# Kernel tuning notes

Measured on AMD Instinct MI355X. Metric: run time of the kernel, lower is better.

The kernel has to match this reference:

```python
import jax, jax.numpy as jnp
import numpy as np

N = 50000   # nodes
E = 800000  # edges
IN = 256    # input feature dim
H = 4       # heads (per layer)
D = 64      # num_hidden per head
C = 16      # n_clusters
NEG = 0.2   # leaky_relu negative slope


def _gat_conv(x, W, attn_l, attn_r, src, dst):
    """DGL GATConv (no residual, no dropout at eval), activation=elu.
    x: [N, F_in], W: [F_in, H*D], attn_l/attn_r: [H, D]. Returns [N, H, D]."""
    feat = (x @ W).reshape(N, H, D)                      # [N,H,D]
    el = jnp.sum(feat * attn_l, axis=-1)                 # [N,H]
    er = jnp.sum(feat * attn_r, axis=-1)                 # [N,H]
    e = jax.nn.leaky_relu(el[src] + er[dst], NEG)        # [E,H]
    # numerically stable segment softmax over incoming edges of each dst node
    emax = jax.ops.segment_max(e, dst, num_segments=N)   # [N,H]
    emax = jnp.where(jnp.isfinite(emax), emax, 0.0)
    ee = jnp.exp(e - emax[dst])                          # [E,H]
    denom = jax.ops.segment_sum(ee, dst, num_segments=N) # [N,H]
    a = ee / jnp.maximum(denom[dst], 1e-9)               # [E,H]
    msg = feat[src] * a[:, :, None]                      # [E,H,D]
    rst = jax.ops.segment_sum(msg, dst, num_segments=N)  # [N,H,D]
    return jax.nn.elu(rst)


def setup_inputs() -> dict:
    key = jax.random.key(0)
    ks = jax.random.split(key, 12)
    def w(k, shape, fan):
        return jax.random.normal(k, shape, jnp.float32) * np.float32(1.0 / np.sqrt(fan))
    return {
        "x": jax.random.normal(ks[0], (N, IN), jnp.float32),
        "src": jax.random.randint(ks[1], (E,), 0, N, jnp.int32),
        "dst": jax.random.randint(ks[2], (E,), 0, N, jnp.int32),
        "W0": w(ks[3], (IN, H * D), IN),
        "al0": w(ks[4], (H, D), D),
        "ar0": w(ks[5], (H, D), D),
        "W1": w(ks[6], (H * D, H * D), H * D),
        "al1": w(ks[7], (H, D), D),
        "ar1": w(ks[8], (H, D), D),
        "Wc": w(ks[9], (D, C), D),
        "bc": jnp.zeros((C,), jnp.float32),
    }


def reference(x, src, dst, W0, al0, ar0, W1, al1, ar1, Wc, bc):
    h = _gat_conv(x, W0, al0, ar0, src, dst)              # [N,H,D]
    h = _gat_conv(h.reshape(N, H * D), W1, al1, ar1, src, dst)
    heads = jnp.transpose(h, (1, 0, 2))                   # [H,N,D]
    # original bug: same cluster layer (index num_layers-1) used for every head
    cs = jax.nn.softmax(jnp.einsum("hnd,dc->hnc", heads, Wc) + bc, axis=-1)  # [H,N,C]
    # pack (heads, cs) into one array along last dim for a single output
    return jnp.concatenate([heads, cs], axis=-1)          # [H,N,D+C]
```

## Files before the change

kernel.cpp:

```cpp
#include <hip/hip_runtime.h>
#include <hip/hip_bf16.h>
#include <math.h>

#define N_NODES 50000
#define N_EDGES 800000
#define NH 4
#define ND 64
#define NF 256
#define NC 16
#define NEG_SLOPE 0.2f

typedef __attribute__((ext_vector_type(8))) short bf16x8;
typedef __attribute__((ext_vector_type(4))) float f32x4;

__device__ __forceinline__ float elu_f(float x) {
    return x > 0.f ? x : (__expf(x) - 1.f);
}

__device__ __forceinline__ ushort bf16_rne(float f) {
    union { float f; unsigned u; } v; v.f = f;
    unsigned u = v.u;
    u += 0x7fffu + ((u >> 16) & 1u);
    return (ushort)(u >> 16);
}

__device__ __forceinline__ float bf2f(ushort u) {
    return __uint_as_float(((unsigned)u) << 16);
}

__global__ __launch_bounds__(256) void cast_bf16_kernel(const float* __restrict__ in,
                                                        ushort* __restrict__ out, int n8) {
    int i = blockIdx.x * 256 + threadIdx.x;
    if (i >= n8) return;
    float4 a = *(const float4*)(in + i * 8);
    float4 b = *(const float4*)(in + i * 8 + 4);
    ushort o[8] = {bf16_rne(a.x), bf16_rne(a.y), bf16_rne(a.z), bf16_rne(a.w),
                   bf16_rne(b.x), bf16_rne(b.y), bf16_rne(b.z), bf16_rne(b.w)};
    *(bf16x8*)(out + i * 8) = *(bf16x8*)o;
}

__global__ __launch_bounds__(256) void castWt_kernel(const float* __restrict__ W0,
                                                     const float* __restrict__ W1,
                                                     ushort* __restrict__ Wt0,
                                                     ushort* __restrict__ Wt1) {
    const float* W = (blockIdx.x < 256) ? W0 : W1;
    ushort* Wt = (blockIdx.x < 256) ? Wt0 : Wt1;
    int n = blockIdx.x & 255;
    int k = threadIdx.x;
    Wt[n * 256 + k] = bf16_rne(W[k * 256 + n]);
}

__global__ __launch_bounds__(256) void gemm_bf16(const ushort* __restrict__ A,
                                                 const ushort* __restrict__ Bt,
                                                 ushort* __restrict__ Cbf,
                                                 const float* __restrict__ al,
                                                 const float* __restrict__ ar,
                                                 float* __restrict__ el,
                                                 float* __restrict__ er, int M) {
    __shared__ __align__(16) ushort As[128 * 64];
    __shared__ __align__(16) ushort Bs[128 * 64];
    const int t = threadIdx.x;
    const int l = t & 63;
    const int w = t >> 6;
    const int wm = (w >> 1) * 64, wn = (w & 1) * 64;
    const int m0 = blockIdx.x * 128, n0 = blockIdx.y * 128;
    const int lr = l & 15, lk = l >> 4;

    f32x4 acc[4][4] = {};
    const int sr = t >> 3;
    const int sc = t & 7;
    const int scw = sc ^ (sr & 7);

    for (int k0 = 0; k0 < 256; k0 += 64) {
        #pragma unroll
        for (int q = 0; q < 4; ++q) {
            int row = q * 32 + sr;
            int ga = min(m0 + row, M - 1);
            bf16x8 va = *(const bf16x8*)(A + (size_t)ga * 256 + k0 + sc * 8);
            *(bf16x8*)(&As[row * 64 + scw * 8]) = va;
            bf16x8 vb = *(const bf16x8*)(Bt + (size_t)(n0 + row) * 256 + k0 + sc * 8);
            *(bf16x8*)(&Bs[row * 64 + scw * 8]) = vb;
        }
        __syncthreads();
        #pragma unroll
        for (int kk = 0; kk < 2; ++kk) {
            bf16x8 af[4], bfr[4];
            #pragma unroll
            for (int mi = 0; mi < 4; ++mi) {
                int row = wm + mi * 16 + lr;
                int kb = kk * 4 + lk;
                af[mi] = *(const bf16x8*)(&As[row * 64 + (kb ^ (row & 7)) * 8]);
            }
            #pragma unroll
            for (int ni = 0; ni < 4; ++ni) {
                int col = wn + ni * 16 + lr;
                int kb = kk * 4 + lk;
                bfr[ni] = *(const bf16x8*)(&Bs[col * 64 + (kb ^ (col & 7)) * 8]);
            }
            #pragma unroll
            for (int mi = 0; mi < 4; ++mi)
                #pragma unroll
                for (int ni = 0; ni < 4; ++ni)
                    acc[mi][ni] = __builtin_amdgcn_mfma_f32_16x16x32_bf16(af[mi], bfr[ni], acc[mi][ni], 0, 0, 0);
        }
        __syncthreads();
    }
    const int h = (n0 + wn) >> 6;
    float alv[4], arv[4];
    #pragma unroll
    for (int ni = 0; ni < 4; ++ni) {
        alv[ni] = al[h * ND + ni * 16 + lr];
        arv[ni] = ar[h * ND + ni * 16 + lr];
    }
    #pragma unroll
    for (int mi = 0; mi < 4; ++mi) {
        #pragma unroll
        for (int j = 0; j < 4; ++j) {
            int row = m0 + wm + mi * 16 + lk * 4 + j;
            float pe = 0.f, pr = 0.f;
            #pragma unroll
            for (int ni = 0; ni < 4; ++ni) {
                float v = acc[mi][ni][j];
                pe += v * alv[ni];
                pr += v * arv[ni];
                if (row < M)
                    Cbf[(size_t)row * 256 + n0 + wn + ni * 16 + lr] = bf16_rne(v);
            }
            #pragma unroll
            for (int m = 1; m <= 8; m <<= 1) {
                pe += __shfl_xor(pe, m, 64);
                pr += __shfl_xor(pr, m, 64);
            }
            if (lr == 0 && row < M) {
                el[row * 4 + h] = pe;
                er[row * 4 + h] = pr;
            }
        }
    }
}

__global__ __launch_bounds__(256) void hist_kernel(const int* __restrict__ dst, int* __restrict__ count) {
    int e = blockIdx.x * 256 + threadIdx.x;
    if (e < N_EDGES) atomicAdd(&count[dst[e]], 1);
}

__global__ __launch_bounds__(256) void scan1_kernel(const int* __restrict__ counts,
                                                    int* __restrict__ offs,
                                                    int* __restrict__ bsums) {
    __shared__ int sh[256];
    int tid = threadIdx.x;
    int i = blockIdx.x * 256 + tid;
    int v = (i < N_NODES) ? counts[i] : 0;
    sh[tid] = v;
    __syncthreads();
    #pragma unroll
    for (int ofs = 1; ofs < 256; ofs <<= 1) {
        int t = (tid >= ofs) ? sh[tid - ofs] : 0;
        __syncthreads();
        sh[tid] += t;
        __syncthreads();
    }
    if (i < N_NODES) offs[i] = sh[tid] - v;
    if (tid == 255) bsums[blockIdx.x] = sh[255];
}

__global__ __launch_bounds__(256) void scan2_kernel(const int* __restrict__ bsums,
                                                    int* __restrict__ boffs, int nb) {
    __shared__ int sh[256];
    int tid = threadIdx.x;
    int v = (tid < nb) ? bsums[tid] : 0;
    sh[tid] = v;
    __syncthreads();
    #pragma unroll
    for (int ofs = 1; ofs < 256; ofs <<= 1) {
        int t = (tid >= ofs) ? sh[tid - ofs] : 0;
        __syncthreads();
        sh[tid] += t;
        __syncthreads();
    }
    if (tid < nb) boffs[tid] = sh[tid] - v;
}

__global__ __launch_bounds__(256) void scan3_kernel(int* __restrict__ offs,
                                                    const int* __restrict__ boffs,
                                                    int* __restrict__ cursor) {
    int i = blockIdx.x * 256 + threadIdx.x;
    if (i < N_NODES) {
        int v = offs[i] + boffs[i >> 8];
        offs[i] = v;
        cursor[i] = v;
    }
    if (i == 0) offs[N_NODES] = N_EDGES;
}

__global__ __launch_bounds__(256) void scatter_kernel(const int* __restrict__ src,
                                                      const int* __restrict__ dst,
                                                      int* __restrict__ cursor,
                                                      int* __restrict__ csrc,
                                                      int* __restrict__ cdst) {
    int e = blockIdx.x * 256 + threadIdx.x;
    if (e >= N_EDGES) return;
    int d = dst[e];
    int p = atomicAdd(&cursor[d], 1);
    csrc[p] = src[e];
    cdst[p] = d;
}

__global__ __launch_bounds__(256) void edge_w_kernel(const int* __restrict__ csrc,
                                                     const int* __restrict__ cdst,
                                                     const float* __restrict__ el,
                                                     const float* __restrict__ er,
                                                     float* __restrict__ w) {
    int i = blockIdx.x * 256 + threadIdx.x;
    if (i >= N_EDGES) return;
    int s = csrc[i], d = cdst[i];
    float4 lv = *(const float4*)(el + s * 4);
    float4 rv = *(const float4*)(er + d * 4);
    float lvv[4] = {lv.x, lv.y, lv.z, lv.w};
    float rvv[4] = {rv.x, rv.y, rv.z, rv.w};
    float o[4];
    #pragma unroll
    for (int hh = 0; hh < 4; ++hh) {
        float v = lvv[hh] + rvv[hh];
        v = v > 0.f ? v : NEG_SLOPE * v;
        o[hh] = __expf(v);
    }
    *(float4*)(w + (size_t)i * 4) = make_float4(o[0], o[1], o[2], o[3]);
}

#define AGG_BATCH16()                                                            \
    for (int i = s0; i < s1; i += 16) {                                          \
        int sid[16]; float wv[16]; ushort4 fr[16];                               \
        _Pragma("unroll")                                                        \
        for (int u = 0; u < 16; ++u) {                                           \
            int idx = (i + u < s1) ? i + u : s1 - 1;                             \
            sid[u] = csrc[idx];                                                  \
            wv[u] = (i + u < s1) ? w[(size_t)idx * 4 + h] : 0.f;                 \
        }                                                                        \
        _Pragma("unroll")                                                        \
        for (int u = 0; u < 16; ++u)                                             \
            fr[u] = *(const ushort4*)(featbf + (size_t)sid[u] * NF + lane * 4);  \
        _Pragma("unroll")                                                        \
        for (int u = 0; u < 16; ++u) {                                           \
            dsum += wv[u];                                                       \
            acc.x += wv[u] * bf2f(fr[u].x);                                      \
            acc.y += wv[u] * bf2f(fr[u].y);                                      \
            acc.z += wv[u] * bf2f(fr[u].z);                                      \
            acc.w += wv[u] * bf2f(fr[u].w);                                      \
        }                                                                        \
    }

__global__ __launch_bounds__(256) void agg_l0_kernel(const ushort* __restrict__ featbf,
                                                     const int* __restrict__ csrc,
                                                     const int* __restrict__ offs,
                                                     const float* __restrict__ w,
                                                     ushort* __restrict__ out_bf) {
    int n = blockIdx.x * 4 + (threadIdx.x >> 6);
    int lane = threadIdx.x & 63;
    int h = lane >> 4;
    int s0 = offs[n], s1 = offs[n + 1];
    float4 acc = make_float4(0.f, 0.f, 0.f, 0.f);
    float dsum = 0.f;
    AGG_BATCH16()
    float inv = 1.f / fmaxf(dsum, 1e-9f);
    ushort o[4] = {bf16_rne(elu_f(acc.x * inv)), bf16_rne(elu_f(acc.y * inv)),
                   bf16_rne(elu_f(acc.z * inv)), bf16_rne(elu_f(acc.w * inv))};
    *(ushort4*)(out_bf + (size_t)n * NF + lane * 4) = *(ushort4*)o;
}

__global__ __launch_bounds__(256) void agg_final_kernel(const ushort* __restrict__ featbf,
                                                        const int* __restrict__ csrc,
                                                        const int* __restrict__ offs,
                                                        const float* __restrict__ w,
                                                        const float* __restrict__ Wc,
                                                        const float* __restrict__ bc,
                                                        float* __restrict__ out) {
    int n = blockIdx.x * 4 + (threadIdx.x >> 6);
    int lane = threadIdx.x & 63;
    int h = lane >> 4;
    int g = lane & 15;
    int s0 = offs[n], s1 = offs[n + 1];
    float4 acc = make_float4(0.f, 0.f, 0.f, 0.f);
    float dsum = 0.f;
    AGG_BATCH16()
    float inv = 1.f / fmaxf(dsum, 1e-9f);
    float v0 = elu_f(acc.x * inv), v1 = elu_f(acc.y * inv);
    float v2 = elu_f(acc.z * inv), v3 = elu_f(acc.w * inv);
    size_t base = (size_t)h * N_NODES * (ND + NC) + (size_t)n * (ND + NC);
    *(float4*)(out + base + g * 4) = make_float4(v0, v1, v2, v3);
    float logit[NC];
    #pragma unroll
    for (int c = 0; c < NC; ++c) {
        int d0 = g * 4;
        float p = v0 * Wc[(d0 + 0) * NC + c] + v1 * Wc[(d0 + 1) * NC + c] +
                  v2 * Wc[(d0 + 2) * NC + c] + v3 * Wc[(d0 + 3) * NC + c];
        p += __shfl_xor(p, 1, 64);
        p += __shfl_xor(p, 2, 64);
        p += __shfl_xor(p, 4, 64);
        p += __shfl_xor(p, 8, 64);
        logit[c] = p + bc[c];
    }
    float m = logit[0];
    #pragma unroll
    for (int c = 1; c < NC; ++c) m = fmaxf(m, logit[c]);
    float ssum = 0.f;
    #pragma unroll
    for (int c = 0; c < NC; ++c) ssum += __expf(logit[c] - m);
    out[base + ND + g] = __expf(logit[g] - m) / ssum;
}

extern "C" void kernel_launch(void* const* d_in, const int* in_sizes, int n_in,
                              void* d_out, int out_size, void* d_ws, size_t ws_size,
                              hipStream_t stream) {
    const float* x   = (const float*)d_in[0];
    const int* src   = (const int*)d_in[1];
    const int* dst   = (const int*)d_in[2];
    const float* W0  = (const float*)d_in[3];
    const float* al0 = (const float*)d_in[4];
    const float* ar0 = (const float*)d_in[5];
    const float* W1  = (const float*)d_in[6];
    const float* al1 = (const float*)d_in[7];
    const float* ar1 = (const float*)d_in[8];
    const float* Wc  = (const float*)d_in[9];
    const float* bc  = (const float*)d_in[10];
    float* out = (float*)d_out;

    char* ws = (char*)d_ws;
    size_t off = 0;
    auto alloc = [&](size_t bytes) { void* p = ws + off; off = (off + bytes + 255) & ~(size_t)255; return p; };
    ushort* featbf = (ushort*)alloc((size_t)N_NODES * NF * 2);
    ushort* xbf    = (ushort*)alloc((size_t)N_NODES * NF * 2);
    ushort* hbuf   = (ushort*)alloc((size_t)N_NODES * NF * 2);
    ushort* Wt0    = (ushort*)alloc((size_t)256 * 256 * 2);
    ushort* Wt1    = (ushort*)alloc((size_t)256 * 256 * 2);
    float*  el     = (float*)alloc((size_t)N_NODES * NH * 4);
    float*  er     = (float*)alloc((size_t)N_NODES * NH * 4);
    float*  wbuf   = (float*)alloc((size_t)N_EDGES * NH * 4);
    int* counts    = (int*)alloc((size_t)N_NODES * 4);
    int* offs      = (int*)alloc((size_t)(N_NODES + 1) * 4);
    int* cursor    = (int*)alloc((size_t)N_NODES * 4);
    int* csrc      = (int*)alloc((size_t)N_EDGES * 4);
    int* cdst      = (int*)alloc((size_t)N_EDGES * 4);
    int* bsums     = (int*)alloc(256 * 4);
    int* boffs     = (int*)alloc(256 * 4);

    const int EB = (N_EDGES + 255) / 256;
    const int NB = (N_NODES + 255) / 256;
    const int GEMM_MB = (N_NODES + 127) / 128;
    const int C8 = (N_NODES * NF / 8 + 255) / 256;

    hipMemsetAsync(counts, 0, (size_t)N_NODES * 4, stream);
    hist_kernel<<<EB, 256, 0, stream>>>(dst, counts);
    scan1_kernel<<<NB, 256, 0, stream>>>(counts, offs, bsums);
    scan2_kernel<<<1, 256, 0, stream>>>(bsums, boffs, NB);
    scan3_kernel<<<NB, 256, 0, stream>>>(offs, boffs, cursor);
    scatter_kernel<<<EB, 256, 0, stream>>>(src, dst, cursor, csrc, cdst);

    castWt_kernel<<<512, 256, 0, stream>>>(W0, W1, Wt0, Wt1);
    cast_bf16_kernel<<<C8, 256, 0, stream>>>(x, xbf, N_NODES * NF / 8);

    gemm_bf16<<<dim3(GEMM_MB, 2), 256, 0, stream>>>(xbf, Wt0, featbf, al0, ar0, el, er, N_NODES);
    edge_w_kernel<<<EB, 256, 0, stream>>>(csrc, cdst, el, er, wbuf);
    agg_l0_kernel<<<N_NODES / 4, 256, 0, stream>>>(featbf, csrc, offs, wbuf, hbuf);

    gemm_bf16<<<dim3(GEMM_MB, 2), 256, 0, stream>>>(hbuf, Wt1, featbf, al1, ar1, el, er, N_NODES);
    edge_w_kernel<<<EB, 256, 0, stream>>>(csrc, cdst, el, er, wbuf);
    agg_final_kernel<<<N_NODES / 4, 256, 0, stream>>>(featbf, csrc, offs, wbuf, Wc, bc, out);
}
```

Before: 380.0 us.

## Stage gathered neighbor feature rows through LDS via global_load_lds in aggregation

The aggregation kernels now gather neighbor feature rows with direct global-to-LDS 16-byte loads instead of per-lane 8-byte register loads. Each instruction fetches two source rows, with half the wave on each row, into a per-wave LDS buffer. The row is then read back from LDS for accumulation. Node index and edge offsets are made wave-uniform with readfirstlane. The aim is wider memory transactions and lower VGPR pressure. The cost is an extra LDS round trip, a full vmcnt(0) wait per chunk, and 32KB of LDS per block, which may reduce occupancy.

```diff
diff --git a/kernel.cpp b/kernel.cpp
--- a/kernel.cpp
+++ b/kernel.cpp
@@ -9,6 +9,7 @@
 #define NF 256
 #define NC 16
 #define NEG_SLOPE 0.2f
+#define AGG_CHUNK 16
 
 typedef __attribute__((ext_vector_type(8))) short bf16x8;
 typedef __attribute__((ext_vector_type(4))) float f32x4;
@@ -26,6 +27,13 @@
 
 __device__ __forceinline__ float bf2f(ushort u) {
     return __uint_as_float(((unsigned)u) << 16);
+}
+
+__device__ __forceinline__ void row_pair_to_lds(const ushort* gp, char* lp) {
+    __builtin_amdgcn_global_load_lds(
+        (const __attribute__((address_space(1))) unsigned int*)gp,
+        (__attribute__((address_space(3))) unsigned int*)lp,
+        16, 0, 0);
 }
 
 __global__ __launch_bounds__(256) void cast_bf16_kernel(const float* __restrict__ in,
@@ -228,26 +236,33 @@
     *(float4*)(w + (size_t)i * 4) = make_float4(o[0], o[1], o[2], o[3]);
 }
 
-#define AGG_BATCH16()                                                            \
-    for (int i = s0; i < s1; i += 16) {                                          \
-        int sid[16]; float wv[16]; ushort4 fr[16];                               \
-        _Pragma("unroll")                                                        \
-        for (int u = 0; u < 16; ++u) {                                           \
-            int idx = (i + u < s1) ? i + u : s1 - 1;                             \
-            sid[u] = csrc[idx];                                                  \
-            wv[u] = (i + u < s1) ? w[(size_t)idx * 4 + h] : 0.f;                 \
-        }                                                                        \
-        _Pragma("unroll")                                                        \
-        for (int u = 0; u < 16; ++u)                                             \
-            fr[u] = *(const ushort4*)(featbf + (size_t)sid[u] * NF + lane * 4);  \
-        _Pragma("unroll")                                                        \
-        for (int u = 0; u < 16; ++u) {                                           \
-            dsum += wv[u];                                                       \
-            acc.x += wv[u] * bf2f(fr[u].x);                                      \
-            acc.y += wv[u] * bf2f(fr[u].y);                                      \
-            acc.z += wv[u] * bf2f(fr[u].z);                                      \
-            acc.w += wv[u] * bf2f(fr[u].w);                                      \
-        }                                                                        \
+#define AGG_STAGE_LOOP()                                                          \
+    for (int i = s0; i < s1; i += AGG_CHUNK) {                                    \
+        int sid[AGG_CHUNK]; float wv[AGG_CHUNK];                                  \
+        _Pragma("unroll")                                                         \
+        for (int u = 0; u < AGG_CHUNK; ++u) {                                     \
+            int sl = i + u;                                                       \
+            int idx = sl < s1 ? sl : s1 - 1;                                      \
+            sid[u] = csrc[idx];                                                   \
+            wv[u] = sl < s1 ? w[(size_t)idx * 4 + h] : 0.f;                       \
+        }                                                                         \
+        _Pragma("unroll")                                                         \
+        for (int u = 0; u < AGG_CHUNK / 2; ++u) {                                 \
+            int s2 = rowsel ? sid[2 * u + 1] : sid[2 * u];                        \
+            const ushort* gp = featbf + (size_t)s2 * NF + bsub * 8;               \
+            row_pair_to_lds(gp, myl + u * 1024);                                  \
+        }                                                                         \
+        asm volatile("s_waitcnt vmcnt(0)" ::: "memory");                          \
+        __builtin_amdgcn_sched_barrier(0);                                        \
+        _Pragma("unroll")                                                         \
+        for (int u = 0; u < AGG_CHUNK; ++u) {                                     \
+            ushort4 fr = *(const ushort4*)(myl + u * 512 + lane * 8);             \
+            dsum += wv[u];                                                        \
+            acc.x += wv[u] * bf2f(fr.x);                                          \
+            acc.y += wv[u] * bf2f(fr.y);                                          \
+            acc.z += wv[u] * bf2f(fr.z);                                          \
+            acc.w += wv[u] * bf2f(fr.w);                                          \
+        }                                                                         \
     }
 
 __global__ __launch_bounds__(256) void agg_l0_kernel(const ushort* __restrict__ featbf,
@@ -255,13 +270,19 @@
                                                      const int* __restrict__ offs,
                                                      const float* __restrict__ w,
                                                      ushort* __restrict__ out_bf) {
-    int n = blockIdx.x * 4 + (threadIdx.x >> 6);
+    __shared__ __align__(16) char ldsbuf[4][AGG_CHUNK * 512];
+    int wid = threadIdx.x >> 6;
+    char* myl = &ldsbuf[wid][0];
+    int n = __builtin_amdgcn_readfirstlane(blockIdx.x * 4 + wid);
     int lane = threadIdx.x & 63;
     int h = lane >> 4;
-    int s0 = offs[n], s1 = offs[n + 1];
+    int rowsel = lane >> 5;
+    int bsub = lane & 31;
+    int s0 = __builtin_amdgcn_readfirstlane(offs[n]);
+    int s1 = __builtin_amdgcn_readfirstlane(offs[n + 1]);
     float4 acc = make_float4(0.f, 0.f, 0.f, 0.f);
     float dsum = 0.f;
-    AGG_BATCH16()
+    AGG_STAGE_LOOP()
     float inv = 1.f / fmaxf(dsum, 1e-9f);
     ushort o[4] = {bf16_rne(elu_f(acc.x * inv)), bf16_rne(elu_f(acc.y * inv)),
                    bf16_rne(elu_f(acc.z * inv)), bf16_rne(elu_f(acc.w * inv))};
@@ -275,14 +296,20 @@
                                                         const float* __restrict__ Wc,
                                                         const float* __restrict__ bc,
                                                         float* __restrict__ out) {
-    int n = blockIdx.x * 4 + (threadIdx.x >> 6);
+    __shared__ __align__(16) char ldsbuf[4][AGG_CHUNK * 512];
+    int wid = threadIdx.x >> 6;
+    char* myl = &ldsbuf[wid][0];
+    int n = __builtin_amdgcn_readfirstlane(blockIdx.x * 4 + wid);
     int lane = threadIdx.x & 63;
     int h = lane >> 4;
     int g = lane & 15;
-    int s0 = offs[n], s1 = offs[n + 1];
+    int rowsel = lane >> 5;
+    int bsub = lane & 31;
+    int s0 = __builtin_amdgcn_readfirstlane(offs[n]);
+    int s1 = __builtin_amdgcn_readfirstlane(offs[n + 1]);
     float4 acc = make_float4(0.f, 0.f, 0.f, 0.f);
     float dsum = 0.f;
-    AGG_BATCH16()
+    AGG_STAGE_LOOP()
     float inv = 1.f / fmaxf(dsum, 1e-9f);
     float v0 = elu_f(acc.x * inv), v1 = elu_f(acc.y * inv);
     float v2 = elu_f(acc.z * inv), v3 = elu_f(acc.w * inv);
```

Measured after the change: 440.1 us. +15.8%, slower.

## Slice feature matrix into 32-column planes for cache-local gather aggregation

Applied to the files above, without the earlier changes.

The GEMM now writes its bf16 output as 8 column slices of 32 features, each stored contiguously per node. Aggregation launches 8 blocks per node group, one per slice, so each block gathers 64-byte rows from a 3.2MB plane that can stay in L2/MALL instead of random 512-byte rows across the full matrix. Within a wave, lanes split into 8 edge groups and partial sums are reduced with shuffles. The cluster softmax is moved to a separate kernel that rereads the output. This costs 8x more index and weight reads, an extra launch and an extra pass over the output.

```diff
diff --git a/kernel.cpp b/kernel.cpp
--- a/kernel.cpp
+++ b/kernel.cpp
@@ -9,6 +9,8 @@
 #define NF 256
 #define NC 16
 #define NEG_SLOPE 0.2f
+#define NSLICE 8
+#define SLICE_W 32
 
 typedef __attribute__((ext_vector_type(8))) short bf16x8;
 typedef __attribute__((ext_vector_type(4))) float f32x4;
@@ -52,7 +54,7 @@
 
 __global__ __launch_bounds__(256) void gemm_bf16(const ushort* __restrict__ A,
                                                  const ushort* __restrict__ Bt,
-                                                 ushort* __restrict__ Cbf,
+                                                 ushort* __restrict__ Cs,
                                                  const float* __restrict__ al,
                                                  const float* __restrict__ ar,
                                                  float* __restrict__ el,
@@ -120,11 +122,12 @@
             float pe = 0.f, pr = 0.f;
             #pragma unroll
             for (int ni = 0; ni < 4; ++ni) {
+                int col = n0 + wn + ni * 16 + lr;
                 float v = acc[mi][ni][j];
                 pe += v * alv[ni];
                 pr += v * arv[ni];
                 if (row < M)
-                    Cbf[(size_t)row * 256 + n0 + wn + ni * 16 + lr] = bf16_rne(v);
+                    Cs[(size_t)(col >> 5) * N_NODES * SLICE_W + (size_t)row * SLICE_W + (col & 31)] = bf16_rne(v);
             }
             #pragma unroll
             for (int m = 1; m <= 8; m <<= 1) {
@@ -228,72 +231,85 @@
     *(float4*)(w + (size_t)i * 4) = make_float4(o[0], o[1], o[2], o[3]);
 }
 
-#define AGG_BATCH16()                                                            \
-    for (int i = s0; i < s1; i += 16) {                                          \
-        int sid[16]; float wv[16]; ushort4 fr[16];                               \
-        _Pragma("unroll")                                                        \
-        for (int u = 0; u < 16; ++u) {                                           \
-            int idx = (i + u < s1) ? i + u : s1 - 1;                             \
-            sid[u] = csrc[idx];                                                  \
-            wv[u] = (i + u < s1) ? w[(size_t)idx * 4 + h] : 0.f;                 \
-        }                                                                        \
-        _Pragma("unroll")                                                        \
-        for (int u = 0; u < 16; ++u)                                             \
-            fr[u] = *(const ushort4*)(featbf + (size_t)sid[u] * NF + lane * 4);  \
-        _Pragma("unroll")                                                        \
-        for (int u = 0; u < 16; ++u) {                                           \
-            dsum += wv[u];                                                       \
-            acc.x += wv[u] * bf2f(fr[u].x);                                      \
-            acc.y += wv[u] * bf2f(fr[u].y);                                      \
-            acc.z += wv[u] * bf2f(fr[u].z);                                      \
-            acc.w += wv[u] * bf2f(fr[u].w);                                      \
-        }                                                                        \
-    }
-
-__global__ __launch_bounds__(256) void agg_l0_kernel(const ushort* __restrict__ featbf,
-                                                     const int* __restrict__ csrc,
-                                                     const int* __restrict__ offs,
-                                                     const float* __restrict__ w,
-                                                     ushort* __restrict__ out_bf) {
-    int n = blockIdx.x * 4 + (threadIdx.x >> 6);
-    int lane = threadIdx.x & 63;
-    int h = lane >> 4;
-    int s0 = offs[n], s1 = offs[n + 1];
-    float4 acc = make_float4(0.f, 0.f, 0.f, 0.f);
-    float dsum = 0.f;
-    AGG_BATCH16()
+#define AGG_SLICE_BODY()                                                           \
+    int b = blockIdx.x;                                                            \
+    int slice = b & 7;                                                             \
+    int wid = threadIdx.x >> 6;                                                    \
+    int n = ((b >> 3) << 2) + wid;                                                 \
+    int lane = threadIdx.x & 63;                                                   \
+    int eg = lane >> 3, fc = lane & 7;                                             \
+    int h = slice >> 1;                                                            \
+    const ushort* base = fs + (size_t)slice * N_NODES * SLICE_W;                   \
+    int s0 = offs[n], s1 = offs[n + 1];                                            \
+    float4 acc = make_float4(0.f, 0.f, 0.f, 0.f);                                  \
+    float dsum = 0.f;                                                              \
+    for (int i = s0; i < s1; i += 16) {                                            \
+        int iA = i + eg, iB = i + 8 + eg;                                          \
+        int idxA = min(iA, s1 - 1), idxB = min(iB, s1 - 1);                        \
+        int sA = csrc[idxA], sB = csrc[idxB];                                      \
+        float wA = iA < s1 ? wbuf[(size_t)idxA * 4 + h] : 0.f;                     \
+        float wB = iB < s1 ? wbuf[(size_t)idxB * 4 + h] : 0.f;                     \
+        ushort4 fA = *(const ushort4*)(base + (size_t)sA * SLICE_W + fc * 4);      \
+        ushort4 fB = *(const ushort4*)(base + (size_t)sB * SLICE_W + fc * 4);      \
+        acc.x += wA * bf2f(fA.x) + wB * bf2f(fB.x);                                \
+        acc.y += wA * bf2f(fA.y) + wB * bf2f(fB.y);                                \
+        acc.z += wA * bf2f(fA.z) + wB * bf2f(fB.z);                                \
+        acc.w += wA * bf2f(fA.w) + wB * bf2f(fB.w);                                \
+        dsum += wA + wB;                                                           \
+    }                                                                              \
+    _Pragma("unroll")                                                              \
+    for (int m = 8; m <= 32; m <<= 1) {                                            \
+        acc.x += __shfl_xor(acc.x, m, 64);                                         \
+        acc.y += __shfl_xor(acc.y, m, 64);                                         \
+        acc.z += __shfl_xor(acc.z, m, 64);                                         \
+        acc.w += __shfl_xor(acc.w, m, 64);                                         \
+        dsum += __shfl_xor(dsum, m, 64);                                           \
+    }                                                                              \
     float inv = 1.f / fmaxf(dsum, 1e-9f);
-    ushort o[4] = {bf16_rne(elu_f(acc.x * inv)), bf16_rne(elu_f(acc.y * inv)),
-                   bf16_rne(elu_f(acc.z * inv)), bf16_rne(elu_f(acc.w * inv))};
-    *(ushort4*)(out_bf + (size_t)n * NF + lane * 4) = *(ushort4*)o;
-}
-
-__global__ __launch_bounds__(256) void agg_final_kernel(const ushort* __restrict__ featbf,
-                                                        const int* __restrict__ csrc,
-                                                        const int* __restrict__ offs,
-                                                        const float* __restrict__ w,
-                                                        const float* __restrict__ Wc,
-                                                        const float* __restrict__ bc,
-                                                        float* __restrict__ out) {
+
+__global__ __launch_bounds__(256) void agg_slice_l0(const ushort* __restrict__ fs,
+                                                    const int* __restrict__ csrc,
+                                                    const int* __restrict__ offs,
+                                                    const float* __restrict__ wbuf,
+                                                    ushort* __restrict__ hbuf) {
+    AGG_SLICE_BODY()
+    if (eg == 0) {
+        ushort o[4] = {bf16_rne(elu_f(acc.x * inv)), bf16_rne(elu_f(acc.y * inv)),
+                       bf16_rne(elu_f(acc.z * inv)), bf16_rne(elu_f(acc.w * inv))};
+        *(ushort4*)(hbuf + (size_t)n * NF + slice * SLICE_W + fc * 4) = *(ushort4*)o;
+    }
+}
+
+__global__ __launch_bounds__(256) void agg_slice_final(const ushort* __restrict__ fs,
+                                                       const int* __restrict__ csrc,
+                                                       const int* __restrict__ offs,
+                                                       const float* __restrict__ wbuf,
+                                                       float* __restrict__ out) {
+    AGG_SLICE_BODY()
+    if (eg == 0) {
+        float4 v = make_float4(elu_f(acc.x * inv), elu_f(acc.y * inv),
+                               elu_f(acc.z * inv), elu_f(acc.w * inv));
+        size_t p = (size_t)h * N_NODES * (ND + NC) + (size_t)n * (ND + NC)
+                 + (slice & 1) * SLICE_W + fc * 4;
+        *(float4*)(out + p) = v;
+    }
+}
+
+__global__ __launch_bounds__(256) void cluster_kernel(const float* __restrict__ Wc,
+                                                      const float* __restrict__ bc,
+                                                      float* __restrict__ out) {
     int n = blockIdx.x * 4 + (threadIdx.x >> 6);
     int lane = threadIdx.x & 63;
     int h = lane >> 4;
     int g = lane & 15;
-    int s0 = offs[n], s1 = offs[n + 1];
-    float4 acc = make_float4(0.f, 0.f, 0.f, 0.f);
-    float dsum = 0.f;
-    AGG_BATCH16()
-    float inv = 1.f / fmaxf(dsum, 1e-9f);
-    float v0 = elu_f(acc.x * inv), v1 = elu_f(acc.y * inv);
-    float v2 = elu_f(acc.z * inv), v3 = elu_f(acc.w * inv);
     size_t base = (size_t)h * N_NODES * (ND + NC) + (size_t)n * (ND + NC);
-    *(float4*)(out + base + g * 4) = make_float4(v0, v1, v2, v3);
+    float4 v = *(const float4*)(out + base + g * 4);
     float logit[NC];
     #pragma unroll
     for (int c = 0; c < NC; ++c) {
         int d0 = g * 4;
-        float p = v0 * Wc[(d0 + 0) * NC + c] + v1 * Wc[(d0 + 1) * NC + c] +
-                  v2 * Wc[(d0 + 2) * NC + c] + v3 * Wc[(d0 + 3) * NC + c];
+        float p = v.x * Wc[(d0 + 0) * NC + c] + v.y * Wc[(d0 + 1) * NC + c] +
+                  v.z * Wc[(d0 + 2) * NC + c] + v.w * Wc[(d0 + 3) * NC + c];
         p += __shfl_xor(p, 1, 64);
         p += __shfl_xor(p, 2, 64);
         p += __shfl_xor(p, 4, 64);
@@ -328,7 +344,7 @@
     char* ws = (char*)d_ws;
     size_t off = 0;
     auto alloc = [&](size_t bytes) { void* p = ws + off; off = (off + bytes + 255) & ~(size_t)255; return p; };
-    ushort* featbf = (ushort*)alloc((size_t)N_NODES * NF * 2);
+    ushort* featsl = (ushort*)alloc((size_t)N_NODES * NF * 2);
     ushort* xbf    = (ushort*)alloc((size_t)N_NODES * NF * 2);
     ushort* hbuf   = (ushort*)alloc((size_t)N_NODES * NF * 2);
     ushort* Wt0    = (ushort*)alloc((size_t)256 * 256 * 2);
@@ -348,6 +364,7 @@
     const int NB = (N_NODES + 255) / 256;
     const int GEMM_MB = (N_NODES + 127) / 128;
     const int C8 = (N_NODES * NF / 8 + 255) / 256;
+    const int AGG_B = (N_NODES / 4) * NSLICE;
 
     hipMemsetAsync(counts, 0, (size_t)N_NODES * 4, stream);
     hist_kernel<<<EB, 256, 0, stream>>>(dst, counts);
@@ -359,11 +376,13 @@
     castWt_kernel<<<512, 256, 0, stream>>>(W0, W1, Wt0, Wt1);
     cast_bf16_kernel<<<C8, 256, 0, stream>>>(x, xbf, N_NODES * NF / 8);
 
-    gemm_bf16<<<dim3(GEMM_MB, 2), 256, 0, stream>>>(xbf, Wt0, featbf, al0, ar0, el, er, N_NODES);
+    gemm_bf16<<<dim3(GEMM_MB, 2), 256, 0, stream>>>(xbf, Wt0, featsl, al0, ar0, el, er, N_NODES);
     edge_w_kernel<<<EB, 256, 0, stream>>>(csrc, cdst, el, er, wbuf);
-    agg_l0_kernel<<<N_NODES / 4, 256, 0, stream>>>(featbf, csrc, offs, wbuf, hbuf);
-
-    gemm_bf16<<<dim3(GEMM_MB, 2), 256, 0, stream>>>(hbuf, Wt1, featbf, al1, ar1, el, er, N_NODES);
+    agg_slice_l0<<<AGG_B, 256, 0, stream>>>(featsl, csrc, offs, wbuf, hbuf);
+
+    gemm_bf16<<<dim3(GEMM_MB, 2), 256, 0, stream>>>(hbuf, Wt1, featsl, al1, ar1, el, er, N_NODES);
     edge_w_kernel<<<EB, 256, 0, stream>>>(csrc, cdst, el, er, wbuf);
-    agg_final_kernel<<<N_NODES / 4, 256, 0, stream>>>(featbf, csrc, offs, wbuf, Wc, bc, out);
-}
+    agg_slice_final<<<AGG_B, 256, 0, stream>>>(featsl, csrc, offs, wbuf, out);
+
+    cluster_kernel<<<N_NODES / 4, 256, 0, stream>>>(Wc, bc, out);
+}
```

After: 511.4 us. +34.6%, slower.
